# Kernel optimization log

Measured on AMD Instinct MI355X. Metric: run time of the kernel, lower is better.

Reference implementation:

```python
import jax, jax.numpy as jnp
import numpy as np


def _init_relative_position_index(window_size: int) -> np.ndarray:
    coords = np.stack(np.meshgrid(np.arange(window_size), np.arange(window_size), indexing='ij'))
    coords_flatten = coords.reshape(2, -1)  # [2, wh*ww]
    rel = coords_flatten[:, :, None] - coords_flatten[:, None, :]  # [2, N, N]
    rel = rel.transpose(1, 2, 0).copy()
    rel[:, :, 0] += window_size - 1
    rel[:, :, 1] += window_size - 1
    rel[:, :, 0] *= 2 * window_size - 1
    return rel.sum(-1)  # [N, N] int


def setup_inputs() -> dict:
    B_, N, C, H, WH, NW = 2048, 49, 512, 16, 7, 64
    key = jax.random.key(0)
    ks = jax.random.split(key, 6)
    x = jax.random.normal(ks[0], (B_, N, C), dtype=jnp.float32)
    qkv_w = jax.random.normal(ks[1], (3 * C, C), dtype=jnp.float32) * 0.02
    qkv_b = jax.random.normal(ks[2], (3 * C,), dtype=jnp.float32) * 0.02
    rp_bias_table = jax.random.normal(ks[3], ((2 * WH - 1) ** 2, H), dtype=jnp.float32) * 0.02
    out_w = jax.random.normal(ks[4], (C, C), dtype=jnp.float32) * 0.02
    out_b = jax.random.normal(ks[5], (C,), dtype=jnp.float32) * 0.02
    rp_index = jnp.asarray(_init_relative_position_index(WH), dtype=jnp.int32)
    mask = jnp.zeros((NW, N, N), dtype=jnp.float32)  # 0/-inf shifted-window mask
    return {"x": x, "qkv_w": qkv_w, "qkv_b": qkv_b, "rp_index": rp_index,
            "rp_bias_table": rp_bias_table, "out_w": out_w, "out_b": out_b,
            "mask": mask, "nw": NW}


def reference(x, qkv_w, qkv_b, rp_index, rp_bias_table, out_w, out_b, mask, nw):
    B_, N, C = x.shape
    h = rp_bias_table.shape[1]
    dh = C // h
    scale = float(dh) ** -0.5

    # QKV projection; weight layout is (h dh 3) x C per the module's note.
    qkv = x @ qkv_w.T + qkv_b                      # [B_, N, 3C]
    qkv = qkv.reshape(B_, N, h, dh, 3)             # [B_, N, h, dh, 3]
    q = qkv[..., 0].transpose(0, 2, 1, 3)          # [B_, h, N, dh]
    k = qkv[..., 1].transpose(0, 2, 1, 3)
    v = qkv[..., 2].transpose(0, 2, 1, 3)

    attn = jnp.einsum('bhnd,bhmd->bhnm', q * scale, k)  # [B_, h, N, N]

    # gather relative position bias: [N*N] -> [N, N, h] -> [h, N, N]
    pb = rp_bias_table[rp_index.reshape(-1)].reshape(N, N, h).transpose(2, 0, 1)
    # NOTE: original adds the bias TWICE (attn += pb; attn += pb[None]); replicate.
    attn = attn + pb[None]
    attn = attn + pb[None]

    nW = mask.shape[0]
    attn = attn.reshape(B_ // nW, nW, h, N, N) + mask[None, :, None]
    attn = attn.reshape(B_, h, N, N)
    attn = jax.nn.softmax(attn, axis=-1)
    # attn_drop = proj_drop = 0.0 -> dropout is identity

    out = jnp.einsum('bhnm,bhmd->bhnd', attn, v)   # [B_, h, N, dh]
    out = out.transpose(0, 2, 1, 3).reshape(B_, N, h * dh)
    out = out @ out_w.T + out_b
    return out
```

## Files before the change

### kernel.cpp

```cpp
#include <hip/hip_runtime.h>
#include <hip/hip_bf16.h>
#include <stdint.h>

typedef short s16x8 __attribute__((ext_vector_type(8)));
typedef float f32x4 __attribute__((ext_vector_type(4)));

#define H_ 16
#define DH 32
#define NTOK 49
#define CDIM 512
#define SCALE 0.17677669529663687f

typedef const __attribute__((address_space(1))) uint32_t* gas_ptr;
typedef __attribute__((address_space(3))) uint32_t* las_ptr;
#define GLL16(g, l) __builtin_amdgcn_global_load_lds((gas_ptr)(g), (las_ptr)(l), 16, 0, 0)

__device__ __forceinline__ short f2bf(float f){
  union { __bf16 h; short s; } u;
  u.h = (__bf16)f;
  return u.s;
}

__device__ __forceinline__ s16x8 pack8(float4 a, float4 b){
  s16x8 r;
  r[0]=f2bf(a.x); r[1]=f2bf(a.y); r[2]=f2bf(a.z); r[3]=f2bf(a.w);
  r[4]=f2bf(b.x); r[5]=f2bf(b.y); r[6]=f2bf(b.z); r[7]=f2bf(b.w);
  return r;
}

__device__ __forceinline__ int xcd_swz(int orig, int nwg){
  int q = nwg >> 3, r = nwg & 7;
  int x = orig & 7, idx = orig >> 3;
  return (x < r ? x*(q+1) : r*(q+1) + (x - r)*q) + idx;
}

__global__ void prep_wq_kernel(const float* __restrict__ w, const float* __restrict__ b,
                               short* __restrict__ wq, float* __restrict__ pb)
{
  int t = blockIdx.x*256 + threadIdx.x;
  int jp = t >> 6, kg = t & 63;
  int s = jp >> 9, h = (jp >> 5) & 15, d = jp & 31;
  int srow = h*96 + d*3 + s;
  float fac = (s == 0) ? SCALE : 1.0f;
  const float* wr = w + (size_t)srow*CDIM + kg*8;
  float4 a = *(const float4*)wr;
  float4 c = *(const float4*)(wr+4);
  a.x*=fac; a.y*=fac; a.z*=fac; a.w*=fac;
  c.x*=fac; c.y*=fac; c.z*=fac; c.w*=fac;
  ((s16x8*)(wq + (size_t)jp*CDIM))[kg] = pack8(a,c);
  if (kg == 0) pb[jp] = b[srow]*fac;
}

__global__ void prep_wo_kernel(const float* __restrict__ w, short* __restrict__ wo)
{
  int t = blockIdx.x*256 + threadIdx.x;
  int j = t >> 6, kg = t & 63;
  const float* wr = w + (size_t)j*CDIM + kg*8;
  float4 a = *(const float4*)wr;
  float4 c = *(const float4*)(wr+4);
  ((s16x8*)(wo + (size_t)j*CDIM))[kg] = pack8(a,c);
}

#define BMSTR 50
#define BMSLAB 2464
__global__ void prep_bm_kernel(const int* __restrict__ idx, const float* __restrict__ tab,
                               const float* __restrict__ mask, float* __restrict__ bm)
{
  int wh = blockIdx.x;
  int w = wh >> 4, h = wh & 15;
  const float* mw = mask + (size_t)w*2401;
  float* o = bm + (size_t)wh*BMSLAB;
  for (int i = threadIdx.x; i < 2401; i += 256){
    int r = i / 49, c = i - r*49;
    o[r*BMSTR + c] = mw[i] + 2.0f*tab[idx[i]*H_ + h];
  }
}

__global__ void cvt_kernel(const float* __restrict__ src, short* __restrict__ dst, int n8)
{
  int i = blockIdx.x*blockDim.x + threadIdx.x;
  int stride = gridDim.x*blockDim.x;
  for (; i < n8; i += stride){
    float4 a = ((const float4*)src)[2*i];
    float4 b = ((const float4*)src)[2*i+1];
    ((s16x8*)dst)[i] = pack8(a,b);
  }
}

template<int EPI>
__global__ __launch_bounds__(256)
void gemm128(const short* __restrict__ A, const short* __restrict__ Bm,
             const float* __restrict__ pb,
             short* __restrict__ Q, short* __restrict__ Kd, short* __restrict__ V,
             float* __restrict__ outF, int ntiles, int nwg, int b0)
{
  __shared__ __align__(16) short As[2][8192];
  __shared__ __align__(16) short Bs[2][8192];
  const int tid = threadIdx.x, w = tid >> 6, l = tid & 63;
  const int wg = xcd_swz(blockIdx.x, nwg);
  const int mt = wg / ntiles, jt = wg % ntiles;
  const int wr = w >> 1, wc = w & 1, lg = l >> 4, lc = l & 15;

  const int srow = w*8 + (l >> 3);
  const int sbyte = ((l & 7) ^ (l >> 3)) << 4;
  const char* gA = (const char*)A  + ((size_t)(mt*128 + srow))*1024 + sbyte;
  const char* gB = (const char*)Bm + ((size_t)(jt*128 + srow))*1024 + sbyte;

  f32x4 acc[4][4];
  #pragma unroll
  for (int i=0;i<4;++i)
    #pragma unroll
    for (int j=0;j<4;++j) acc[i][j] = (f32x4){0.f,0.f,0.f,0.f};

  #pragma unroll
  for (int i=0;i<4;++i){
    GLL16(gA + i*32768, (char*)As[0] + i*4096 + w*1024);
    GLL16(gB + i*32768, (char*)Bs[0] + i*4096 + w*1024);
  }

  int buf = 0;
  for (int kt=0; kt<8; ++kt){
    if (kt < 7){
      const char* ga2 = gA + (kt+1)*128;
      const char* gb2 = gB + (kt+1)*128;
      #pragma unroll
      for (int i=0;i<4;++i){
        GLL16(ga2 + i*32768, (char*)As[buf^1] + i*4096 + w*1024);
        GLL16(gb2 + i*32768, (char*)Bs[buf^1] + i*4096 + w*1024);
      }
      asm volatile("s_waitcnt vmcnt(8)" ::: "memory");
    } else {
      asm volatile("s_waitcnt vmcnt(0)" ::: "memory");
    }
    __builtin_amdgcn_s_barrier();

    const char* pA = (const char*)As[buf];
    const char* pB = (const char*)Bs[buf];
    #pragma unroll
    for (int kk=0; kk<2; ++kk){
      const int kbyte = (kk*64 + lg*16) ^ ((lc & 7) << 4);
      s16x8 af[4], bf_[4];
      #pragma unroll
      for (int i=0;i<4;++i)
        af[i]  = *(const s16x8*)(pA + (wr*64 + i*16 + lc)*128 + kbyte);
      #pragma unroll
      for (int j=0;j<4;++j)
        bf_[j] = *(const s16x8*)(pB + (wc*64 + j*16 + lc)*128 + kbyte);
      __builtin_amdgcn_s_setprio(1);
      #pragma unroll
      for (int i=0;i<4;++i)
        #pragma unroll
        for (int j=0;j<4;++j)
          acc[i][j] = __builtin_amdgcn_mfma_f32_16x16x32_bf16(af[i], bf_[j], acc[i][j], 0,0,0);
      __builtin_amdgcn_s_setprio(0);
    }
    __builtin_amdgcn_s_barrier();
    buf ^= 1;
  }

  const int cb = jt*128 + wc*64;
  if (EPI == 0){
    const int s_sel = cb >> 9;
    short* dst = (s_sel==0) ? Q : (s_sel==1 ? Kd : V);
    float bv[4]; int hj[4], dj[4];
    #pragma unroll
    for (int j=0;j<4;++j){
      int cc = cb + j*16 + lc;
      bv[j] = pb[cc];
      hj[j] = (cc >> 5) & 15;
      dj[j] = cc & 31;
    }
    #pragma unroll
    for (int i=0;i<4;++i){
      #pragma unroll
      for (int r=0;r<4;++r){
        int grow = mt*128 + wr*64 + i*16 + lg*4 + r;
        int bl = grow / 49;
        int n  = grow - bl*49;
        #pragma unroll
        for (int j=0;j<4;++j)
          dst[(((size_t)bl*H_ + hj[j])*NTOK + n)*DH + dj[j]] = f2bf(acc[i][j][r] + bv[j]);
      }
    }
  } else {
    float bv[4];
    #pragma unroll
    for (int j=0;j<4;++j) bv[j] = pb[cb + j*16 + lc];
    #pragma unroll
    for (int i=0;i<4;++i){
      #pragma unroll
      for (int r=0;r<4;++r){
        int grow = mt*128 + wr*64 + i*16 + lg*4 + r;
        size_t o = ((size_t)(b0*NTOK) + grow)*CDIM + cb;
        #pragma unroll
        for (int j=0;j<4;++j)
          outF[o + j*16 + lc] = acc[i][j][r] + bv[j];
      }
    }
  }
}

template<int GROUPED>
__global__ __launch_bounds__(256)
void attn_kernel(const short* __restrict__ Q, const short* __restrict__ Kt,
                 const short* __restrict__ V, const float* __restrict__ bm,
                 short* __restrict__ AO, int b0, int nW)
{
  __shared__ __align__(16) short P[4][64][72];
  __shared__ __align__(16) float bmL[BMSLAB];
  const int tid = threadIdx.x, wv = tid >> 6, lane = tid & 63;
  const int lg = lane >> 4, lc = lane & 15;
  const int h = blockIdx.x & 15, rest = blockIdx.x >> 4;

  int bl, widx;
  if (GROUPED){
    widx = rest % nW;
    int g4 = rest / nW;
    bl = widx + (g4*4 + wv)*nW;
  } else {
    bl = rest*4 + wv;
    widx = (b0 + bl) % nW;
  }

  const short* q = Q  + ((size_t)bl*H_ + h)*NTOK*DH;
  const short* k = Kt + ((size_t)bl*H_ + h)*NTOK*DH;
  const short* v = V  + ((size_t)bl*H_ + h)*NTOK*DH;

  if (GROUPED){
    const float4* bmg = (const float4*)(bm + ((size_t)widx*H_ + h)*BMSLAB);
    #pragma unroll
    for (int i=0;i<3;++i){
      int s = tid + i*256;
      if (s < BMSLAB/4) ((float4*)bmL)[s] = bmg[s];
    }
  }

  s16x8 qa[4], kb[4];
  #pragma unroll
  for (int t=0;t<4;++t){
    int r = t*16 + lc; if (r > 48) r = 48;
    qa[t] = *(const s16x8*)(q + r*DH + lg*8);
    kb[t] = *(const s16x8*)(k + r*DH + lg*8);
  }
  f32x4 S[4][4];
  #pragma unroll
  for (int i=0;i<4;++i)
    #pragma unroll
    for (int j=0;j<4;++j) S[i][j] = (f32x4){0.f,0.f,0.f,0.f};
  #pragma unroll
  for (int i=0;i<4;++i)
    #pragma unroll
    for (int j=0;j<4;++j)
      S[i][j] = __builtin_amdgcn_mfma_f32_16x16x32_bf16(qa[i], kb[j], S[i][j], 0,0,0);

  if (GROUPED) __syncthreads();
  const float* bmh = GROUPED ? bmL : (bm + ((size_t)widx*H_ + h)*BMSLAB);

  float rinv[4][4];
  #pragma unroll
  for (int i=0;i<4;++i){
    #pragma unroll
    for (int r=0;r<4;++r){
      int row = i*16 + lg*4 + r;
      float mx = -3.0e38f;
      #pragma unroll
      for (int j=0;j<4;++j){
        int col = j*16 + lc;
        float sv = S[i][j][r];
        if (row < 49 && col < 49) sv += bmh[row*BMSTR+col];
        else sv = -1.0e30f;
        S[i][j][r] = sv;
        mx = fmaxf(mx, sv);
      }
      #pragma unroll
      for (int off=1; off<16; off<<=1) mx = fmaxf(mx, __shfl_xor(mx, off, 64));
      float sum = 0.f;
      #pragma unroll
      for (int j=0;j<4;++j){
        float e = __expf(S[i][j][r] - mx);
        S[i][j][r] = e;
        sum += e;
      }
      #pragma unroll
      for (int off=1; off<16; off<<=1) sum += __shfl_xor(sum, off, 64);
      rinv[i][r] = 1.0f / sum;
    }
  }

  #pragma unroll
  for (int i=0;i<4;++i)
    #pragma unroll
    for (int j=0;j<4;++j)
      #pragma unroll
      for (int r=0;r<4;++r)
        P[wv][i*16 + lg*4 + r][j*16 + lc] = f2bf(S[i][j][r]);

  s16x8 vb[2][2];
  #pragma unroll
  for (int kt=0;kt<2;++kt)
    #pragma unroll
    for (int nt=0;nt<2;++nt){
      s16x8 t;
      #pragma unroll
      for (int e=0;e<8;++e){
        int kk = kt*32 + lg*8 + e; if (kk > 48) kk = 48;
        t[e] = v[kk*DH + nt*16 + lc];
      }
      vb[kt][nt] = t;
    }
  f32x4 O[4][2];
  #pragma unroll
  for (int i=0;i<4;++i){ O[i][0] = (f32x4){0.f,0.f,0.f,0.f}; O[i][1] = (f32x4){0.f,0.f,0.f,0.f}; }
  #pragma unroll
  for (int i=0;i<4;++i){
    #pragma unroll
    for (int kt=0;kt<2;++kt){
      s16x8 pa = *(const s16x8*)&P[wv][i*16 + lc][kt*32 + lg*8];
      #pragma unroll
      for (int nt=0;nt<2;++nt)
        O[i][nt] = __builtin_amdgcn_mfma_f32_16x16x32_bf16(pa, vb[kt][nt], O[i][nt], 0,0,0);
    }
  }
  #pragma unroll
  for (int i=0;i<4;++i)
    #pragma unroll
    for (int r=0;r<4;++r){
      int row = i*16 + lg*4 + r;
      if (row < 49){
        size_t o = ((size_t)bl*NTOK + row)*CDIM + h*DH;
        float rv = rinv[i][r];
        AO[o + lc]      = f2bf(O[i][0][r]*rv);
        AO[o + 16 + lc] = f2bf(O[i][1][r]*rv);
      }
    }
}

extern "C" void kernel_launch(void* const* d_in, const int* in_sizes, int n_in,
                              void* d_out, int out_size, void* d_ws, size_t ws_size,
                              hipStream_t stream)
{
  const float* x      = (const float*)d_in[0];
  const float* qkv_w  = (const float*)d_in[1];
  const float* qkv_b  = (const float*)d_in[2];
  const int*   rp_idx = (const int*)d_in[3];
  const float* rp_tab = (const float*)d_in[4];
  const float* out_w  = (const float*)d_in[5];
  const float* out_b  = (const float*)d_in[6];
  const float* mask   = (const float*)d_in[7];
  const int nW = in_sizes[7] / (NTOK*NTOK);
  float* out = (float*)d_out;

  char* base = (char*)d_ws;
  size_t off = 0;
  auto alloc = [&](size_t bytes)->char*{
    char* p = base + off;
    off = (off + bytes + 255) & ~(size_t)255;
    return p;
  };
  float* bm  = (float*)alloc((size_t)nW*H_*BMSLAB*4);
  short* wq  = (short*)alloc((size_t)1536*CDIM*2);
  float* pbq = (float*)alloc(1536*4);
  short* wo  = (short*)alloc((size_t)CDIM*CDIM*2);

  int CB = 1024;
  while (CB > 128){
    size_t need = off + 5*(size_t)CB*50176;
    if (need <= ws_size) break;
    CB >>= 1;
  }
  short* xb = (short*)alloc((size_t)CB*50176);
  short* Q  = (short*)alloc((size_t)CB*50176);
  short* K  = (short*)alloc((size_t)CB*50176);
  short* V  = (short*)alloc((size_t)CB*50176);
  short* AO = (short*)alloc((size_t)CB*50176);

  hipLaunchKernelGGL(prep_bm_kernel, dim3(nW*H_), dim3(256), 0, stream,
                     rp_idx, rp_tab, mask, bm);
  hipLaunchKernelGGL(prep_wq_kernel, dim3(1536*64/256), dim3(256), 0, stream,
                     qkv_w, qkv_b, wq, pbq);
  hipLaunchKernelGGL(prep_wo_kernel, dim3(512*64/256), dim3(256), 0, stream,
                     out_w, wo);

  const bool grouped = (CB % (4*nW)) == 0;
  const int nchunk = 2048 / CB;
  const int mtiles = CB*NTOK/128;
  const int n8 = CB*3136;
  for (int c=0; c<nchunk; ++c){
    int b0 = c*CB;
    hipLaunchKernelGGL(cvt_kernel, dim3(2048), dim3(256), 0, stream,
                       x + (size_t)b0*NTOK*CDIM, xb, n8);
    hipLaunchKernelGGL((gemm128<0>), dim3(mtiles*12), dim3(256), 0, stream,
                       xb, wq, pbq, Q, K, V, (float*)nullptr, 12, mtiles*12, b0);
    if (grouped)
      hipLaunchKernelGGL((attn_kernel<1>), dim3(CB*4), dim3(256), 0, stream,
                         Q, K, V, bm, AO, b0, nW);
    else
      hipLaunchKernelGGL((attn_kernel<0>), dim3(CB*4), dim3(256), 0, stream,
                         Q, K, V, bm, AO, b0, nW);
    hipLaunchKernelGGL((gemm128<1>), dim3(mtiles*4), dim3(256), 0, stream,
                       AO, wo, out_b, (short*)nullptr, (short*)nullptr, (short*)nullptr,
                       out, 4, mtiles*4, b0);
  }
}
```

Before: 573.5 us.

## Fuse fp32-to-bf16 conversion into QKV GEMM and store V transposed

Removes the separate cvt kernel by having the QKV GEMM load fp32 x through registers, pack it to bf16 and write it into a single swizzled LDS buffer, while B is still double-buffered through global_load_lds. The V output is written transposed and padded to 64 columns, so the attention kernel loads V fragments as vectors instead of gathering scalars. The chunk size is halved to 512 and the workspace is resized. This saves a full HBM round trip of the activation copy, but adds register pressure and a single-buffered A path with an extra barrier; the padded V^T columns are left unwritten.

```diff
diff --git a/kernel.cpp b/kernel.cpp
--- a/kernel.cpp
+++ b/kernel.cpp
@@ -76,23 +76,132 @@
   }
 }
 
-__global__ void cvt_kernel(const float* __restrict__ src, short* __restrict__ dst, int n8)
-{
-  int i = blockIdx.x*blockDim.x + threadIdx.x;
-  int stride = gridDim.x*blockDim.x;
-  for (; i < n8; i += stride){
-    float4 a = ((const float4*)src)[2*i];
-    float4 b = ((const float4*)src)[2*i+1];
-    ((s16x8*)dst)[i] = pack8(a,b);
-  }
-}
-
-template<int EPI>
+__global__ __launch_bounds__(256, 3)
+void qkv_gemm(const float* __restrict__ xf, const short* __restrict__ Bm,
+              const float* __restrict__ pb,
+              short* __restrict__ Q, short* __restrict__ Kd, short* __restrict__ VT,
+              int ntiles, int nwg)
+{
+  __shared__ __align__(16) short As[8192];
+  __shared__ __align__(16) short Bs[2][8192];
+  const int tid = threadIdx.x, w = tid >> 6, l = tid & 63;
+  const int wg = xcd_swz(blockIdx.x, nwg);
+  const int mt = wg / ntiles, jt = wg % ntiles;
+  const int wr = w >> 1, wc = w & 1, lg = l >> 4, lc = l & 15;
+
+  const int srow = w*8 + (l >> 3);
+  const int sbyte = ((l & 7) ^ (l >> 3)) << 4;
+  const char* gB = (const char*)Bm + ((size_t)(jt*128 + srow))*1024 + sbyte;
+
+  const int arow = tid >> 1, ah = tid & 1;
+  const float* gA = xf + ((size_t)(mt*128 + arow))*CDIM + ah*32;
+  const int awb = arow*128;
+  const int asw = (arow & 7) << 4;
+
+  f32x4 acc[4][4];
+  #pragma unroll
+  for (int i=0;i<4;++i)
+    #pragma unroll
+    for (int j=0;j<4;++j) acc[i][j] = (f32x4){0.f,0.f,0.f,0.f};
+
+  float4 rA[8];
+  #pragma unroll
+  for (int i=0;i<4;++i) GLL16(gB + i*32768, (char*)Bs[0] + i*4096 + w*1024);
+  {
+    const float4* p = (const float4*)gA;
+    #pragma unroll
+    for (int i=0;i<8;++i) rA[i] = p[i];
+  }
+  #pragma unroll
+  for (int i=0;i<4;++i) GLL16(gB + 128 + i*32768, (char*)Bs[1] + i*4096 + w*1024);
+
+  #pragma unroll
+  for (int kt=0; kt<8; ++kt){
+    if (kt < 7){ asm volatile("s_waitcnt vmcnt(4)" ::: "memory"); }
+    else       { asm volatile("s_waitcnt vmcnt(0)" ::: "memory"); }
+
+    {
+      s16x8 s0 = pack8(rA[0], rA[1]);
+      s16x8 s1 = pack8(rA[2], rA[3]);
+      s16x8 s2 = pack8(rA[4], rA[5]);
+      s16x8 s3 = pack8(rA[6], rA[7]);
+      char* ab = (char*)As + awb;
+      *(s16x8*)(ab + ((ah*64 +  0) ^ asw)) = s0;
+      *(s16x8*)(ab + ((ah*64 + 16) ^ asw)) = s1;
+      *(s16x8*)(ab + ((ah*64 + 32) ^ asw)) = s2;
+      *(s16x8*)(ab + ((ah*64 + 48) ^ asw)) = s3;
+    }
+    if (kt < 7){
+      const float4* p = (const float4*)(gA + (kt+1)*64);
+      #pragma unroll
+      for (int i=0;i<8;++i) rA[i] = p[i];
+    }
+    asm volatile("s_waitcnt lgkmcnt(0)" ::: "memory");
+    __builtin_amdgcn_s_barrier();
+
+    const char* pA = (const char*)As;
+    const char* pB = (const char*)Bs[kt & 1];
+    #pragma unroll
+    for (int kk=0; kk<2; ++kk){
+      const int kbyte = (kk*64 + lg*16) ^ ((lc & 7) << 4);
+      s16x8 af[4], bf_[4];
+      #pragma unroll
+      for (int i=0;i<4;++i)
+        af[i]  = *(const s16x8*)(pA + (wr*64 + i*16 + lc)*128 + kbyte);
+      #pragma unroll
+      for (int j=0;j<4;++j)
+        bf_[j] = *(const s16x8*)(pB + (wc*64 + j*16 + lc)*128 + kbyte);
+      __builtin_amdgcn_s_setprio(1);
+      #pragma unroll
+      for (int i=0;i<4;++i)
+        #pragma unroll
+        for (int j=0;j<4;++j)
+          acc[i][j] = __builtin_amdgcn_mfma_f32_16x16x32_bf16(af[i], bf_[j], acc[i][j], 0,0,0);
+      __builtin_amdgcn_s_setprio(0);
+    }
+    __builtin_amdgcn_s_barrier();
+    if (kt < 6){
+      #pragma unroll
+      for (int i=0;i<4;++i)
+        GLL16(gB + (kt+2)*128 + i*32768, (char*)Bs[kt & 1] + i*4096 + w*1024);
+    }
+  }
+
+  const int cb = jt*128 + wc*64;
+  const int s_sel = cb >> 9;
+  float bv[4]; int hj[4], dj[4];
+  #pragma unroll
+  for (int j=0;j<4;++j){
+    int cc = cb + j*16 + lc;
+    bv[j] = pb[cc];
+    hj[j] = (cc >> 5) & 15;
+    dj[j] = cc & 31;
+  }
+  #pragma unroll
+  for (int i=0;i<4;++i){
+    #pragma unroll
+    for (int r=0;r<4;++r){
+      int grow = mt*128 + wr*64 + i*16 + lg*4 + r;
+      int bl = grow / 49;
+      int n  = grow - bl*49;
+      if (s_sel == 2){
+        #pragma unroll
+        for (int j=0;j<4;++j)
+          VT[(((size_t)bl*H_ + hj[j])*DH + dj[j])*64 + n] = f2bf(acc[i][j][r] + bv[j]);
+      } else {
+        short* dst = (s_sel==0) ? Q : Kd;
+        #pragma unroll
+        for (int j=0;j<4;++j)
+          dst[(((size_t)bl*H_ + hj[j])*NTOK + n)*DH + dj[j]] = f2bf(acc[i][j][r] + bv[j]);
+      }
+    }
+  }
+}
+
 __global__ __launch_bounds__(256)
-void gemm128(const short* __restrict__ A, const short* __restrict__ Bm,
-             const float* __restrict__ pb,
-             short* __restrict__ Q, short* __restrict__ Kd, short* __restrict__ V,
-             float* __restrict__ outF, int ntiles, int nwg, int b0)
+void proj_gemm(const short* __restrict__ A, const short* __restrict__ Bm,
+               const float* __restrict__ pb, float* __restrict__ outF,
+               int ntiles, int nwg, int b0)
 {
   __shared__ __align__(16) short As[2][8192];
   __shared__ __align__(16) short Bs[2][8192];
@@ -159,43 +268,18 @@
   }
 
   const int cb = jt*128 + wc*64;
-  if (EPI == 0){
-    const int s_sel = cb >> 9;
-    short* dst = (s_sel==0) ? Q : (s_sel==1 ? Kd : V);
-    float bv[4]; int hj[4], dj[4];
-    #pragma unroll
-    for (int j=0;j<4;++j){
-      int cc = cb + j*16 + lc;
-      bv[j] = pb[cc];
-      hj[j] = (cc >> 5) & 15;
-      dj[j] = cc & 31;
-    }
-    #pragma unroll
-    for (int i=0;i<4;++i){
-      #pragma unroll
-      for (int r=0;r<4;++r){
-        int grow = mt*128 + wr*64 + i*16 + lg*4 + r;
-        int bl = grow / 49;
-        int n  = grow - bl*49;
-        #pragma unroll
-        for (int j=0;j<4;++j)
-          dst[(((size_t)bl*H_ + hj[j])*NTOK + n)*DH + dj[j]] = f2bf(acc[i][j][r] + bv[j]);
-      }
-    }
-  } else {
-    float bv[4];
-    #pragma unroll
-    for (int j=0;j<4;++j) bv[j] = pb[cb + j*16 + lc];
-    #pragma unroll
-    for (int i=0;i<4;++i){
-      #pragma unroll
-      for (int r=0;r<4;++r){
-        int grow = mt*128 + wr*64 + i*16 + lg*4 + r;
-        size_t o = ((size_t)(b0*NTOK) + grow)*CDIM + cb;
-        #pragma unroll
-        for (int j=0;j<4;++j)
-          outF[o + j*16 + lc] = acc[i][j][r] + bv[j];
-      }
+  float bv[4];
+  #pragma unroll
+  for (int j=0;j<4;++j) bv[j] = pb[cb + j*16 + lc];
+  #pragma unroll
+  for (int i=0;i<4;++i){
+    #pragma unroll
+    for (int r=0;r<4;++r){
+      int grow = mt*128 + wr*64 + i*16 + lg*4 + r;
+      size_t o = ((size_t)(b0*NTOK) + grow)*CDIM + cb;
+      #pragma unroll
+      for (int j=0;j<4;++j)
+        outF[o + j*16 + lc] = acc[i][j][r] + bv[j];
     }
   }
 }
@@ -203,7 +287,7 @@
 template<int GROUPED>
 __global__ __launch_bounds__(256)
 void attn_kernel(const short* __restrict__ Q, const short* __restrict__ Kt,
-                 const short* __restrict__ V, const float* __restrict__ bm,
+                 const short* __restrict__ VT, const float* __restrict__ bm,
                  short* __restrict__ AO, int b0, int nW)
 {
   __shared__ __align__(16) short P[4][64][72];
@@ -222,9 +306,9 @@
     widx = (b0 + bl) % nW;
   }
 
-  const short* q = Q  + ((size_t)bl*H_ + h)*NTOK*DH;
-  const short* k = Kt + ((size_t)bl*H_ + h)*NTOK*DH;
-  const short* v = V  + ((size_t)bl*H_ + h)*NTOK*DH;
+  const short* q  = Q  + ((size_t)bl*H_ + h)*NTOK*DH;
+  const short* k  = Kt + ((size_t)bl*H_ + h)*NTOK*DH;
+  const short* vt = VT + ((size_t)bl*H_ + h)*DH*64;
 
   if (GROUPED){
     const float4* bmg = (const float4*)(bm + ((size_t)widx*H_ + h)*BMSLAB);
@@ -299,15 +383,9 @@
   #pragma unroll
   for (int kt=0;kt<2;++kt)
     #pragma unroll
-    for (int nt=0;nt<2;++nt){
-      s16x8 t;
-      #pragma unroll
-      for (int e=0;e<8;++e){
-        int kk = kt*32 + lg*8 + e; if (kk > 48) kk = 48;
-        t[e] = v[kk*DH + nt*16 + lc];
-      }
-      vb[kt][nt] = t;
-    }
+    for (int nt=0;nt<2;++nt)
+      vb[kt][nt] = *(const s16x8*)(vt + (nt*16 + lc)*64 + kt*32 + lg*8);
+
   f32x4 O[4][2];
   #pragma unroll
   for (int i=0;i<4;++i){ O[i][0] = (f32x4){0.f,0.f,0.f,0.f}; O[i][1] = (f32x4){0.f,0.f,0.f,0.f}; }
@@ -362,16 +440,15 @@
   float* pbq = (float*)alloc(1536*4);
   short* wo  = (short*)alloc((size_t)CDIM*CDIM*2);
 
-  int CB = 1024;
+  int CB = 512;
   while (CB > 128){
-    size_t need = off + 5*(size_t)CB*50176;
+    size_t need = off + (size_t)CB*(3*50176 + 65536);
     if (need <= ws_size) break;
     CB >>= 1;
   }
-  short* xb = (short*)alloc((size_t)CB*50176);
   short* Q  = (short*)alloc((size_t)CB*50176);
   short* K  = (short*)alloc((size_t)CB*50176);
-  short* V  = (short*)alloc((size_t)CB*50176);
+  short* VT = (short*)alloc((size_t)CB*65536);
   short* AO = (short*)alloc((size_t)CB*50176);
 
   hipLaunchKernelGGL(prep_bm_kernel, dim3(nW*H_), dim3(256), 0, stream,
@@ -384,21 +461,18 @@
   const bool grouped = (CB % (4*nW)) == 0;
   const int nchunk = 2048 / CB;
   const int mtiles = CB*NTOK/128;
-  const int n8 = CB*3136;
   for (int c=0; c<nchunk; ++c){
     int b0 = c*CB;
-    hipLaunchKernelGGL(cvt_kernel, dim3(2048), dim3(256), 0, stream,
-                       x + (size_t)b0*NTOK*CDIM, xb, n8);
-    hipLaunchKernelGGL((gemm128<0>), dim3(mtiles*12), dim3(256), 0, stream,
-                       xb, wq, pbq, Q, K, V, (float*)nullptr, 12, mtiles*12, b0);
+    hipLaunchKernelGGL(qkv_gemm, dim3(mtiles*12), dim3(256), 0, stream,
+                       x + (size_t)b0*NTOK*CDIM, wq, pbq, Q, K, VT,
+                       12, mtiles*12);
     if (grouped)
       hipLaunchKernelGGL((attn_kernel<1>), dim3(CB*4), dim3(256), 0, stream,
-                         Q, K, V, bm, AO, b0, nW);
+                         Q, K, VT, bm, AO, b0, nW);
     else
       hipLaunchKernelGGL((attn_kernel<0>), dim3(CB*4), dim3(256), 0, stream,
-                         Q, K, V, bm, AO, b0, nW);
-    hipLaunchKernelGGL((gemm128<1>), dim3(mtiles*4), dim3(256), 0, stream,
-                       AO, wo, out_b, (short*)nullptr, (short*)nullptr, (short*)nullptr,
-                       out, 4, mtiles*4, b0);
-  }
-}
+                         Q, K, VT, bm, AO, b0, nW);
+    hipLaunchKernelGGL(proj_gemm, dim3(mtiles*4), dim3(256), 0, stream,
+                       AO, wo, out_b, out, 4, mtiles*4, b0);
+  }
+}
```

Measured after the change: 782.5 us. +36.5%, slower.
